# Performance work log

Measured on AMD Instinct MI355X. Metric: run time of the kernel, lower is better.

Reference implementation:

```python
import jax, jax.numpy as jnp
import numpy as np

LN_EPS = 1e-5
NEG_INF = -1e9

def _layer_norm(x, w, b):
    mu = jnp.mean(x, axis=-1, keepdims=True)
    var = jnp.mean(jnp.square(x - mu), axis=-1, keepdims=True)
    return (x - mu) * jax.lax.rsqrt(var + LN_EPS) * w + b

def _mha(q, k, v, wq, wk, wv, wo, mask, num_heads):
    # q: [B,Lq,D], k/v: [B,Lk,D]; weights stored as [in,out]
    B, Lq, D = q.shape
    Lk = k.shape[1]
    dh = D // num_heads
    Q = (q @ wq).reshape(B, Lq, num_heads, dh)
    K = (k @ wk).reshape(B, Lk, num_heads, dh)
    V = (v @ wv).reshape(B, Lk, num_heads, dh)
    scores = jnp.einsum('bqhd,bkhd->bhqk', Q, K) / jnp.sqrt(jnp.asarray(dh, q.dtype))
    if mask is not None:
        scores = jnp.where(mask, NEG_INF, scores)  # mask True = forbidden
    A = jax.nn.softmax(scores, axis=-1)
    out = jnp.einsum('bhqk,bkhd->bqhd', A, V).reshape(B, Lq, D)
    return out @ wo

def setup_inputs() -> dict:
    key = jax.random.key(0)
    B, L, Lm, D, F = 4, 1024, 1024, 1024, 4096
    ks = jax.random.split(key, 12)
    s = 0.02
    inp = {
        'tgt': jax.random.normal(ks[0], (B, L, D), jnp.float32),
        'memory': jax.random.normal(ks[1], (B, Lm, D), jnp.float32),
        'tgt_padding_mask': jnp.zeros((B, L), bool),
        'memory_padding_mask': jnp.zeros((B, Lm), bool),
        'sa_wq': jax.random.normal(ks[2], (D, D), jnp.float32) * s,
        'sa_wk': jax.random.normal(ks[3], (D, D), jnp.float32) * s,
        'sa_wv': jax.random.normal(ks[4], (D, D), jnp.float32) * s,
        'sa_wo': jax.random.normal(ks[5], (D, D), jnp.float32) * s,
        'ca_wq': jax.random.normal(ks[6], (D, D), jnp.float32) * s,
        'ca_wk': jax.random.normal(ks[7], (D, D), jnp.float32) * s,
        'ca_wv': jax.random.normal(ks[8], (D, D), jnp.float32) * s,
        'ca_wo': jax.random.normal(ks[9], (D, D), jnp.float32) * s,
        'ffn_w1': jax.random.normal(ks[10], (D, F), jnp.float32) * s,
        'ffn_b1': jnp.zeros((F,), jnp.float32),
        'ffn_w2': jax.random.normal(ks[11], (F, D), jnp.float32) * s,
        'ffn_b2': jnp.zeros((D,), jnp.float32),
        'ln1_w': jnp.ones((D,), jnp.float32), 'ln1_b': jnp.zeros((D,), jnp.float32),
        'ln2_w': jnp.ones((D,), jnp.float32), 'ln2_b': jnp.zeros((D,), jnp.float32),
        'ln3_w': jnp.ones((D,), jnp.float32), 'ln3_b': jnp.zeros((D,), jnp.float32),
    }
    return inp

def reference(tgt, memory, tgt_padding_mask, memory_padding_mask,
              sa_wq, sa_wk, sa_wv, sa_wo,
              ca_wq, ca_wk, ca_wv, ca_wo,
              ffn_w1, ffn_b1, ffn_w2, ffn_b2,
              ln1_w, ln1_b, ln2_w, ln2_b, ln3_w, ln3_b):
    NUM_HEADS = 16
    B, L, D = tgt.shape
    causal = jnp.triu(jnp.ones((L, L), bool), k=1)  # True = forbidden
    attn_mask = causal[None, None, :, :] | tgt_padding_mask[:, None, None, :]
    x = _mha(tgt, tgt, tgt, sa_wq, sa_wk, sa_wv, sa_wo, attn_mask, NUM_HEADS)
    tgt = _layer_norm(tgt + x, ln1_w, ln1_b)
    mem_mask = memory_padding_mask[:, None, None, :]
    x = _mha(tgt, memory, memory, ca_wq, ca_wk, ca_wv, ca_wo, mem_mask, NUM_HEADS)
    tgt = _layer_norm(tgt + x, ln2_w, ln2_b)
    h = jax.nn.gelu(tgt @ ffn_w1 + ffn_b1)
    ffn_out = h @ ffn_w2 + ffn_b2
    return _layer_norm(tgt + ffn_out, ln3_w, ln3_b)
```

## Files before the change

kernel.cpp:

```cpp
#include <hip/hip_runtime.h>
#include <cstdint>
#include <cstddef>


using u16 = unsigned short;
typedef float f32x4 __attribute__((ext_vector_type(4)));
typedef __bf16 bf16x8 __attribute__((ext_vector_type(8)));

__device__ inline float bf2f(u16 h) { return __uint_as_float(((unsigned)h) << 16); }
__device__ inline u16 f2bf(float f) {
  unsigned u = __float_as_uint(f);
  u += 0x7fffu + ((u >> 16) & 1u);
  return (u16)(u >> 16);
}

__device__ inline void gload16(const void* g, void* l) {
  __builtin_amdgcn_global_load_lds(
      (__attribute__((address_space(1))) void*)g,
      (__attribute__((address_space(3))) void*)l, 16, 0, 0);
}

template <int N>
__device__ inline void waitv() {
  if constexpr (N == 0)      asm volatile("s_waitcnt vmcnt(0)" ::: "memory");
  else if constexpr (N == 4) asm volatile("s_waitcnt vmcnt(4)" ::: "memory");
  else if constexpr (N == 6) asm volatile("s_waitcnt vmcnt(6)" ::: "memory");
  else if constexpr (N == 8) asm volatile("s_waitcnt vmcnt(8)" ::: "memory");
}
template <int N>
__device__ inline void waitl() {
  if constexpr (N == 0)      asm volatile("s_waitcnt lgkmcnt(0)" ::: "memory");
  else if constexpr (N == 4) asm volatile("s_waitcnt lgkmcnt(4)" ::: "memory");
  else if constexpr (N == 8) asm volatile("s_waitcnt lgkmcnt(8)" ::: "memory");
}
__device__ inline void sbar() {
  __builtin_amdgcn_s_barrier();
  __builtin_amdgcn_sched_barrier(0);
}

__device__ inline float gelu_tanh(float x) {
  float u = 0.7978845608028654f * (x + 0.044715f * x * x * x);
  u = fminf(fmaxf(u, -10.f), 10.f);
  float e = __expf(2.0f * u);
  float t = (e - 1.0f) / (e + 1.0f);
  return 0.5f * x * (1.0f + t);
}

__global__ __launch_bounds__(256) void fill_sentinel(float* __restrict__ out,
                                                     float val, int n) {
  int i = blockIdx.x * 1024 + threadIdx.x;
#pragma unroll
  for (int j = 0; j < 4; j++)
    if (i + j * 256 < n) out[i + j * 256] = val;
}

__global__ __launch_bounds__(256) void cast_bf16(const float* __restrict__ S,
                                                 u16* __restrict__ D) {
  int i = (blockIdx.x * 256 + threadIdx.x) * 8;
  float4 a = *(const float4*)&S[i];
  float4 b = *(const float4*)&S[i + 4];
  union { u16 h[8]; uint4 v; } p;
  p.h[0] = f2bf(a.x); p.h[1] = f2bf(a.y); p.h[2] = f2bf(a.z); p.h[3] = f2bf(a.w);
  p.h[4] = f2bf(b.x); p.h[5] = f2bf(b.y); p.h[6] = f2bf(b.z); p.h[7] = f2bf(b.w);
  *(uint4*)&D[i] = p.v;
}

__global__ __launch_bounds__(256) void transpose_w(const float* __restrict__ S,
                                                   u16* __restrict__ D, int K,
                                                   int N) {
  __shared__ float t[32][33];
  int bx = blockIdx.x * 32, by = blockIdx.y * 32;
  int tx = threadIdx.x & 31, ty = threadIdx.x >> 5;
  for (int i = ty; i < 32; i += 8)
    t[i][tx] = S[(size_t)(by + i) * N + bx + tx];
  __syncthreads();
  for (int i = ty; i < 32; i += 8)
    D[(size_t)(bx + i) * K + by + tx] = f2bf(t[tx][i]);
}

__global__ __launch_bounds__(256) void transpose_v(const u16* __restrict__ S,
                                                   int stride,
                                                   u16* __restrict__ VT, int L) {
  __shared__ u16 t[32][33];
  int bh = blockIdx.z, b = bh >> 4, h = bh & 15;
  int l0 = blockIdx.x * 32, d0 = blockIdx.y * 32;
  int tx = threadIdx.x & 31, ty = threadIdx.x >> 5;
  const u16* Sp = S + (size_t)(b * L) * stride + h * 64;
  for (int i = ty; i < 32; i += 8)
    t[i][tx] = Sp[(size_t)(l0 + i) * stride + d0 + tx];
  __syncthreads();
  for (int i = ty; i < 32; i += 8)
    VT[((size_t)bh * 64 + d0 + i) * L + l0 + tx] = t[tx][i];
}

template <int EPI>
__global__ __launch_bounds__(512) void gemm_8ph(
    const u16* __restrict__ A, int lda, const u16* __restrict__ Bt,
    u16* __restrict__ C, int ldc, const float* __restrict__ bias, int K) {
  constexpr int BK = 64;
  __shared__ __attribute__((aligned(16))) u16 As[2][256 * BK];
  __shared__ __attribute__((aligned(16))) u16 Bs[2][256 * BK];
  const int tid = threadIdx.x;
  const int lane = tid & 63, w = tid >> 6;
  const int wr = (w >> 2) * 128, wc = (w & 3) * 64;
  const int ml = lane & 15, quad = lane >> 4;

  const int nwg = gridDim.x * gridDim.y;
  const int orig = blockIdx.x + blockIdx.y * gridDim.x;
  const int wg = (orig & 7) * (nwg >> 3) + (orig >> 3);
  const int bx = wg % gridDim.x, by = wg / gridDim.x;
  const int bm = by * 256, bn = bx * 256;

  const u16* Bb = Bt + (size_t)bn * K;
  const int srow = tid >> 3;
  const int scol = ((tid & 7) ^ (srow & 7)) * 8;

  auto stgA = [&](int t, int h) {
    const int buf = t & 1, k0 = t * BK;
#pragma unroll
    for (int r = 0; r < 2; r++)
      gload16(&A[(size_t)(bm + h * 128 + r * 64 + srow) * lda + k0 + scol],
              &As[buf][(h * 128 + r * 64) * BK + w * 512]);
  };
  auto stgB = [&](int t, int h) {
    const int buf = t & 1, k0 = t * BK;
#pragma unroll
    for (int r = 0; r < 2; r++)
      gload16(&Bb[(size_t)(h * 128 + r * 64 + srow) * K + k0 + scol],
              &Bs[buf][(h * 128 + r * 64) * BK + w * 512]);
  };
  auto ldsA = [&](int buf, int row, int ks) -> bf16x8 {
    return *(const bf16x8*)&As[buf][row * BK + (((ks * 4 + quad) ^ (row & 7)) * 8)];
  };
  auto ldsB = [&](int buf, int row, int ks) -> bf16x8 {
    return *(const bf16x8*)&Bs[buf][row * BK + (((ks * 4 + quad) ^ (row & 7)) * 8)];
  };

  f32x4 acc[8][4] = {};
  const int nk = K / BK;

  stgA(0, 0); stgA(0, 1); stgB(0, 0); stgB(0, 1); stgA(1, 0); stgA(1, 1);
  waitv<4>();
  sbar();

  for (int t = 0; t < nk; t++) {
    const int cur = t & 1;
    bf16x8 aq0[8], aq1[8], bq[4];

#pragma unroll
    for (int i = 0; i < 4; i++)
#pragma unroll
      for (int ks = 0; ks < 2; ks++)
        aq0[i * 2 + ks] = ldsA(cur, wr + i * 16 + ml, ks);
#pragma unroll
    for (int j = 0; j < 2; j++)
#pragma unroll
      for (int ks = 0; ks < 2; ks++)
        bq[j * 2 + ks] = ldsB(cur, wc + j * 16 + ml, ks);
    if (t + 1 < nk) stgB(t + 1, 0);
    __builtin_amdgcn_s_barrier();
    waitl<0>();
    __builtin_amdgcn_sched_barrier(0);
    __builtin_amdgcn_s_setprio(1);
#pragma unroll
    for (int ks = 0; ks < 2; ks++)
#pragma unroll
      for (int i = 0; i < 4; i++)
#pragma unroll
        for (int j = 0; j < 2; j++)
          acc[i][j] = __builtin_amdgcn_mfma_f32_16x16x32_bf16(
              aq0[i * 2 + ks], bq[j * 2 + ks], acc[i][j], 0, 0, 0);
    __builtin_amdgcn_s_setprio(0);
    sbar();

#pragma unroll
    for (int i = 0; i < 4; i++)
#pragma unroll
      for (int ks = 0; ks < 2; ks++)
        aq1[i * 2 + ks] = ldsA(cur, wr + 64 + i * 16 + ml, ks);
    if (t + 1 < nk) stgB(t + 1, 1);
    __builtin_amdgcn_s_barrier();
    waitl<0>();
    __builtin_amdgcn_sched_barrier(0);
    __builtin_amdgcn_s_setprio(1);
#pragma unroll
    for (int ks = 0; ks < 2; ks++)
#pragma unroll
      for (int i = 0; i < 4; i++)
#pragma unroll
        for (int j = 0; j < 2; j++)
          acc[4 + i][j] = __builtin_amdgcn_mfma_f32_16x16x32_bf16(
              aq1[i * 2 + ks], bq[j * 2 + ks], acc[4 + i][j], 0, 0, 0);
    __builtin_amdgcn_s_setprio(0);
    sbar();

#pragma unroll
    for (int j = 0; j < 2; j++)
#pragma unroll
      for (int ks = 0; ks < 2; ks++)
        bq[j * 2 + ks] = ldsB(cur, wc + 32 + j * 16 + ml, ks);
    if (t + 2 < nk) stgA(t + 2, 0);
    __builtin_amdgcn_s_barrier();
    waitl<0>();
    __builtin_amdgcn_sched_barrier(0);
    __builtin_amdgcn_s_setprio(1);
#pragma unroll
    for (int ks = 0; ks < 2; ks++)
#pragma unroll
      for (int i = 0; i < 4; i++)
#pragma unroll
        for (int j = 0; j < 2; j++)
          acc[4 + i][2 + j] = __builtin_amdgcn_mfma_f32_16x16x32_bf16(
              aq1[i * 2 + ks], bq[j * 2 + ks], acc[4 + i][2 + j], 0, 0, 0);
    __builtin_amdgcn_s_setprio(0);
    sbar();

    if (t + 2 < nk) {
      stgA(t + 2, 1);
      waitv<4>();
    } else if (t + 1 < nk) {
      waitv<0>();
    }
    sbar();
    __builtin_amdgcn_s_setprio(1);
#pragma unroll
    for (int ks = 0; ks < 2; ks++)
#pragma unroll
      for (int i = 0; i < 4; i++)
#pragma unroll
        for (int j = 0; j < 2; j++)
          acc[i][2 + j] = __builtin_amdgcn_mfma_f32_16x16x32_bf16(
              aq0[i * 2 + ks], bq[j * 2 + ks], acc[i][2 + j], 0, 0, 0);
    __builtin_amdgcn_s_setprio(0);
    sbar();
  }

#pragma unroll
  for (int i = 0; i < 8; i++)
#pragma unroll
    for (int j = 0; j < 4; j++)
#pragma unroll
      for (int r = 0; r < 4; r++) {
        int row = bm + wr + i * 16 + quad * 4 + r;
        int col = bn + wc + j * 16 + ml;
        float v = acc[i][j][r];
        if (bias) v += bias[col];
        if (EPI == 1) v = gelu_tanh(v);
        C[(size_t)row * ldc + col] = f2bf(v);
      }
}

template <int EPI, int BM, int BN, int WM, int WN>
__global__ __launch_bounds__(512) void gemm_big(
    const u16* __restrict__ A, int lda, const u16* __restrict__ Bt,
    u16* __restrict__ C, int ldc, const float* __restrict__ bias, int K) {
  constexpr int BK = 64;
  constexpr int WTM = BM / WM, WTN = BN / WN;
  constexpr int MR = WTM / 16, NR = WTN / 16;
  constexpr int RPR = 64;
  constexpr int AR = BM / RPR, BR = BN / RPR;
  constexpr int GPT = AR + BR;
  __shared__ __attribute__((aligned(16))) u16 As[2][BM * BK];
  __shared__ __attribute__((aligned(16))) u16 Bs[2][BN * BK];
  const int tid = threadIdx.x;
  const int lane = tid & 63, w = tid >> 6;
  const int wr = (w / WN) * WTM, wc = (w % WN) * WTN;
  const int ml = lane & 15, quad = lane >> 4;

  const int nwg = gridDim.x * gridDim.y;
  const int orig = blockIdx.x + blockIdx.y * gridDim.x;
  const int wg = (orig & 7) * (nwg >> 3) + (orig >> 3);
  const int bx = wg % gridDim.x, by = wg / gridDim.x;
  const int bm = by * BM, bn = bx * BN;

  const u16* Bb = Bt + (size_t)bn * K;
  const int srow = tid >> 3;
  const int scol = ((tid & 7) ^ (srow & 7)) * 8;

  auto stage = [&](int t, int buf) {
    const int k0 = t * BK;
#pragma unroll
    for (int r = 0; r < AR; r++)
      gload16(&A[(size_t)(bm + r * RPR + srow) * lda + k0 + scol],
              &As[buf][r * RPR * BK + w * 512]);
#pragma unroll
    for (int r = 0; r < BR; r++)
      gload16(&Bb[(size_t)(r * RPR + srow) * K + k0 + scol],
              &Bs[buf][r * RPR * BK + w * 512]);
  };
  auto ldsA = [&](int buf, int row, int ks) -> bf16x8 {
    return *(const bf16x8*)&As[buf][row * BK + (((ks * 4 + quad) ^ (row & 7)) * 8)];
  };
  auto ldsB = [&](int buf, int row, int ks) -> bf16x8 {
    return *(const bf16x8*)&Bs[buf][row * BK + (((ks * 4 + quad) ^ (row & 7)) * 8)];
  };

  f32x4 acc[MR][NR] = {};
  const int nk = K / BK;
  stage(0, 0);
  for (int t = 0; t < nk; t++) {
    const int cur = t & 1;
    if (t + 1 < nk) {
      stage(t + 1, cur ^ 1);
      waitv<GPT>();
    } else {
      waitv<0>();
    }
    __builtin_amdgcn_s_barrier();
    __builtin_amdgcn_sched_barrier(0);

    bf16x8 af0[MR], af1[MR], bf0[NR], bf1[NR];
#pragma unroll
    for (int j = 0; j < NR; j++) bf0[j] = ldsB(cur, wc + j * 16 + ml, 0);
#pragma unroll
    for (int i = 0; i < MR; i++) af0[i] = ldsA(cur, wr + i * 16 + ml, 0);
#pragma unroll
    for (int j = 0; j < NR; j++) bf1[j] = ldsB(cur, wc + j * 16 + ml, 1);
#pragma unroll
    for (int i = 0; i < MR; i++) af1[i] = ldsA(cur, wr + i * 16 + ml, 1);
    waitl<MR + NR>();
    __builtin_amdgcn_sched_barrier(0);
    __builtin_amdgcn_s_setprio(1);
#pragma unroll
    for (int i = 0; i < MR; i++)
#pragma unroll
      for (int j = 0; j < NR; j++)
        acc[i][j] = __builtin_amdgcn_mfma_f32_16x16x32_bf16(af0[i], bf0[j], acc[i][j], 0, 0, 0);
    __builtin_amdgcn_s_setprio(0);
    waitl<0>();
    __builtin_amdgcn_sched_barrier(0);
    __builtin_amdgcn_s_setprio(1);
#pragma unroll
    for (int i = 0; i < MR; i++)
#pragma unroll
      for (int j = 0; j < NR; j++)
        acc[i][j] = __builtin_amdgcn_mfma_f32_16x16x32_bf16(af1[i], bf1[j], acc[i][j], 0, 0, 0);
    __builtin_amdgcn_s_setprio(0);

    __builtin_amdgcn_s_barrier();
    __builtin_amdgcn_sched_barrier(0);
  }

#pragma unroll
  for (int i = 0; i < MR; i++)
#pragma unroll
    for (int j = 0; j < NR; j++)
#pragma unroll
      for (int r = 0; r < 4; r++) {
        int row = bm + wr + i * 16 + quad * 4 + r;
        int col = bn + wc + j * 16 + ml;
        float v = acc[i][j][r];
        if (bias) v += bias[col];
        if (EPI == 1) v = gelu_tanh(v);
        C[(size_t)row * ldc + col] = f2bf(v);
      }
}

template <int EPI, int BN, int BK>
__global__ __launch_bounds__(256) void gemm_sm(
    const u16* __restrict__ A, int lda, const u16* __restrict__ Bt,
    u16* __restrict__ C, int ldc, const float* __restrict__ bias, int K) {
  constexpr int ACCN = BN / 32;
  constexpr int CPR = BK / 8, CM = CPR - 1;
  constexpr int RPR = 2048 / BK;
  constexpr int AR = 128 / RPR, BR = BN / RPR;
  __shared__ __attribute__((aligned(16))) u16 As[2][128 * BK];
  __shared__ __attribute__((aligned(16))) u16 Bs[2][BN * BK];
  const int tid = threadIdx.x;
  const int lane = tid & 63, w = tid >> 6;
  const int wr = (BN == 128) ? (w >> 1) * 64 : (w & 1) * 64;
  const int wc = (BN == 128) ? (w & 1) * 64 : (w >> 1) * 32;
  const int ml = lane & 15, quad = lane >> 4;

  const int nwg = gridDim.x * gridDim.y;
  const int orig = blockIdx.x + blockIdx.y * gridDim.x;
  const int wg = (orig & 7) * (nwg >> 3) + (orig >> 3);
  const int bx = wg % gridDim.x, by = wg / gridDim.x;
  const int bm = by * 128, bn = bx * BN;

  const u16* Bb = Bt + (size_t)bn * K;
  const int srow = tid / CPR;
  const int skey = ((srow * BK) >> 6) & CM;
  const int scol = ((tid % CPR) ^ skey) * 8;

  auto stage = [&](int k0, int buf) {
#pragma unroll
    for (int r = 0; r < AR; r++)
      gload16(&A[(size_t)(bm + r * RPR + srow) * lda + k0 + scol],
              &As[buf][r * RPR * BK + w * 512]);
#pragma unroll
    for (int r = 0; r < BR; r++)
      gload16(&Bb[(size_t)(r * RPR + srow) * K + k0 + scol],
              &Bs[buf][r * RPR * BK + w * 512]);
  };

  f32x4 acc[4][ACCN] = {};
  const int nk = K / BK;
  stage(0, 0);
  for (int t = 0; t < nk; t++) {
    const int cur = t & 1;
    __syncthreads();
    if (t + 1 < nk) stage((t + 1) * BK, cur ^ 1);
#pragma unroll
    for (int kk = 0; kk < BK; kk += 32) {
      bf16x8 af[4], bfr[ACCN];
#pragma unroll
      for (int i = 0; i < 4; i++) {
        const int row = wr + i * 16 + ml;
        const int p = ((quad + (kk >> 3)) ^ (((row * BK) >> 6) & CM)) * 8;
        af[i] = *(const bf16x8*)&As[cur][row * BK + p];
      }
#pragma unroll
      for (int j = 0; j < ACCN; j++) {
        const int row = wc + j * 16 + ml;
        const int p = ((quad + (kk >> 3)) ^ (((row * BK) >> 6) & CM)) * 8;
        bfr[j] = *(const bf16x8*)&Bs[cur][row * BK + p];
      }
#pragma unroll
      for (int i = 0; i < 4; i++)
#pragma unroll
        for (int j = 0; j < ACCN; j++)
          acc[i][j] = __builtin_amdgcn_mfma_f32_16x16x32_bf16(af[i], bfr[j],
                                                              acc[i][j], 0, 0, 0);
    }
  }

#pragma unroll
  for (int i = 0; i < 4; i++)
#pragma unroll
    for (int j = 0; j < ACCN; j++)
#pragma unroll
      for (int r = 0; r < 4; r++) {
        int row = bm + wr + i * 16 + quad * 4 + r;
        int col = bn + wc + j * 16 + ml;
        float v = acc[i][j][r];
        if (bias) v += bias[col];
        if (EPI == 1) v = gelu_tanh(v);
        C[(size_t)row * ldc + col] = f2bf(v);
      }
}

#define ATS 72
__global__ __launch_bounds__(256) void attn(
    const u16* __restrict__ Qb, int qstride, const u16* __restrict__ Kb,
    int kstride, const u16* __restrict__ VT, u16* __restrict__ Ob, int ostride,
    int L, int causal) {
  __shared__ __attribute__((aligned(16))) u16 Qs[64 * ATS];
  __shared__ __attribute__((aligned(16))) u16 Ks[64 * ATS];
  __shared__ __attribute__((aligned(16))) u16 Vs[64 * ATS];
  __shared__ __attribute__((aligned(16))) u16 Ps[4][16 * ATS];
  int tid = threadIdx.x, lane = tid & 63, w = tid >> 6;
  int ml = lane & 15, quad = lane >> 4;
  const int nwg = gridDim.x * gridDim.y;
  const int orig = blockIdx.x + blockIdx.y * gridDim.x;
  const int wg = (orig & 7) * (nwg >> 3) + (orig >> 3);
  int qt = wg % gridDim.x, bh = wg / gridDim.x;
  int b = bh >> 4, h = bh & 15;
  const u16* Qp = Qb + (size_t)(b * L) * qstride + h * 64;
  const u16* Kp = Kb + (size_t)(b * L) * kstride + h * 64;
  const u16* Vp = VT + (size_t)bh * 64 * L;

  {
    int r = tid >> 3, cg = (tid & 7) * 8;
    *(uint4*)&Qs[r * ATS + cg] =
        *(const uint4*)&Qp[(size_t)(qt * 64 + r) * qstride + cg];
    *(uint4*)&Qs[(r + 32) * ATS + cg] =
        *(const uint4*)&Qp[(size_t)(qt * 64 + r + 32) * qstride + cg];
  }

  const int r0 = tid >> 3, cg = (tid & 7) * 8;
  uint4 rk0, rk1, rv0, rv1;
  auto issueKV = [&](int kt) {
    rk0 = *(const uint4*)&Kp[(size_t)(kt * 64 + r0) * kstride + cg];
    rk1 = *(const uint4*)&Kp[(size_t)(kt * 64 + r0 + 32) * kstride + cg];
    rv0 = *(const uint4*)&Vp[(size_t)r0 * L + kt * 64 + cg];
    rv1 = *(const uint4*)&Vp[(size_t)(r0 + 32) * L + kt * 64 + cg];
  };
  auto storeKV = [&]() {
    *(uint4*)&Ks[r0 * ATS + cg] = rk0;
    *(uint4*)&Ks[(r0 + 32) * ATS + cg] = rk1;
    *(uint4*)&Vs[r0 * ATS + cg] = rv0;
    *(uint4*)&Vs[(r0 + 32) * ATS + cg] = rv1;
  };

  __syncthreads();
  bf16x8 aq0 = *(const bf16x8*)&Qs[(w * 16 + ml) * ATS + quad * 8];
  bf16x8 aq1 = *(const bf16x8*)&Qs[(w * 16 + ml) * ATS + 32 + quad * 8];

  float lrow[4] = {0.f, 0.f, 0.f, 0.f};
  f32x4 oacc[4] = {};
  int qbase = qt * 64 + w * 16 + quad * 4;

  int ktend = causal ? qt : (L / 64 - 1);
  issueKV(0);
  for (int kt = 0; kt <= ktend; kt++) {
    storeKV();
    __syncthreads();
    if (kt < ktend) issueKV(kt + 1);

    f32x4 sacc[4] = {};
#pragma unroll
    for (int t = 0; t < 4; t++) {
      bf16x8 bk0 = *(const bf16x8*)&Ks[(t * 16 + ml) * ATS + quad * 8];
      bf16x8 bk1 = *(const bf16x8*)&Ks[(t * 16 + ml) * ATS + 32 + quad * 8];
      sacc[t] = __builtin_amdgcn_mfma_f32_16x16x32_bf16(aq0, bk0, sacc[t], 0, 0, 0);
      sacc[t] = __builtin_amdgcn_mfma_f32_16x16x32_bf16(aq1, bk1, sacc[t], 0, 0, 0);
    }
#pragma unroll
    for (int t = 0; t < 4; t++)
#pragma unroll
      for (int r = 0; r < 4; r++) {
        bool masked = causal && (kt * 64 + t * 16 + ml > qbase + r);
        float p = masked ? 0.f : __expf(sacc[t][r] * 0.125f - 11.0f);
        sacc[t][r] = p;
        lrow[r] += p;
      }
    u16* Pw = &Ps[w][0];
#pragma unroll
    for (int t = 0; t < 4; t++)
#pragma unroll
      for (int r = 0; r < 4; r++)
        Pw[(quad * 4 + r) * ATS + t * 16 + ml] = f2bf(sacc[t][r]);
    __syncthreads();
    bf16x8 ap0 = *(const bf16x8*)&Pw[ml * ATS + quad * 8];
    bf16x8 ap1 = *(const bf16x8*)&Pw[ml * ATS + 32 + quad * 8];
#pragma unroll
    for (int t = 0; t < 4; t++) {
      bf16x8 bv0 = *(const bf16x8*)&Vs[(t * 16 + ml) * ATS + quad * 8];
      bf16x8 bv1 = *(const bf16x8*)&Vs[(t * 16 + ml) * ATS + 32 + quad * 8];
      oacc[t] = __builtin_amdgcn_mfma_f32_16x16x32_bf16(ap0, bv0, oacc[t], 0, 0, 0);
      oacc[t] = __builtin_amdgcn_mfma_f32_16x16x32_bf16(ap1, bv1, oacc[t], 0, 0, 0);
    }
    __syncthreads();
  }

#pragma unroll
  for (int r = 0; r < 4; r++) {
    float l = lrow[r];
    l += __shfl_xor(l, 1);
    l += __shfl_xor(l, 2);
    l += __shfl_xor(l, 4);
    l += __shfl_xor(l, 8);
    lrow[r] = l;
  }
#pragma unroll
  for (int r = 0; r < 4; r++) {
    float inv = 1.0f / fmaxf(lrow[r], 1e-37f);
#pragma unroll
    for (int t = 0; t < 4; t++)
      Ob[(size_t)(b * L + qbase + r) * ostride + h * 64 + t * 16 + ml] =
          f2bf(oacc[t][r] * inv);
  }
}

__global__ __launch_bounds__(256) void add_ln(
    const u16* __restrict__ base16, const float* __restrict__ base32,
    const u16* __restrict__ delta, const float* __restrict__ lw,
    const float* __restrict__ lb, u16* __restrict__ out16,
    float* __restrict__ out32) {
  const int D = 1024;
  int row = blockIdx.x;
  float v[4], s = 0.f, s2 = 0.f;
#pragma unroll
  for (int i = 0; i < 4; i++) {
    int c = threadIdx.x + i * 256;
    size_t idx = (size_t)row * D + c;
    float bse = base32 ? base32[idx] : bf2f(base16[idx]);
    float x = bse + bf2f(delta[idx]);
    v[i] = x; s += x; s2 += x * x;
  }
  for (int off = 32; off >= 1; off >>= 1) {
    s += __shfl_xor(s, off);
    s2 += __shfl_xor(s2, off);
  }
  __shared__ float red[8];
  int wid = threadIdx.x >> 6, lane = threadIdx.x & 63;
  if (lane == 0) { red[wid] = s; red[4 + wid] = s2; }
  __syncthreads();
  s = red[0] + red[1] + red[2] + red[3];
  s2 = red[4] + red[5] + red[6] + red[7];
  float mu = s * (1.0f / 1024.0f);
  float var = s2 * (1.0f / 1024.0f) - mu * mu;
  float rs = rsqrtf(fmaxf(var, 0.f) + 1e-5f);
#pragma unroll
  for (int i = 0; i < 4; i++) {
    int c = threadIdx.x + i * 256;
    size_t idx = (size_t)row * D + c;
    float y = (v[i] - mu) * rs * lw[c] + lb[c];
    if (out16) out16[idx] = f2bf(y);
    if (out32) out32[idx] = y;
  }
}

extern "C" void kernel_launch(void* const* d_in, const int* in_sizes, int n_in,
                              void* d_out, int out_size, void* d_ws,
                              size_t ws_size, hipStream_t stream) {
  const int L = 1024;
  const size_t MB = 1ull << 20;
  dim3 blk(256);
  dim3 blk512(512);

  if (ws_size < 64 * MB) {
    fill_sentinel<<<(out_size + 1023) / 1024, blk, 0, stream>>>(
        (float*)d_out, 1000.0f + (float)(ws_size >> 20), out_size);
    return;
  }

  const float* tgt = (const float*)d_in[0];
  const float* memv = (const float*)d_in[1];
  const float* sa_wq = (const float*)d_in[4];
  const float* sa_wk = (const float*)d_in[5];
  const float* sa_wv = (const float*)d_in[6];
  const float* sa_wo = (const float*)d_in[7];
  const float* ca_wq = (const float*)d_in[8];
  const float* ca_wk = (const float*)d_in[9];
  const float* ca_wv = (const float*)d_in[10];
  const float* ca_wo = (const float*)d_in[11];
  const float* ffn_w1 = (const float*)d_in[12];
  const float* ffn_b1 = (const float*)d_in[13];
  const float* ffn_w2 = (const float*)d_in[14];
  const float* ffn_b2 = (const float*)d_in[15];
  const float* ln1w = (const float*)d_in[16];
  const float* ln1b = (const float*)d_in[17];
  const float* ln2w = (const float*)d_in[18];
  const float* ln2b = (const float*)d_in[19];
  const float* ln3w = (const float*)d_in[20];
  const float* ln3b = (const float*)d_in[21];

  const size_t Mu = 1024 * 1024;
  char* base = (char*)d_ws;
  u16* Wt = (u16*)base;
  u16* sa_qkv_t = Wt;
  u16* sa_o_t = Wt + 3 * Mu;
  u16* ca_q_t = Wt + 4 * Mu;
  u16* ca_kv_t = Wt + 5 * Mu;
  u16* ca_o_t = Wt + 7 * Mu;
  u16* ffn1_t = Wt;
  u16* ffn2_t = Wt + 4 * Mu;
  u16* QKV = (u16*)(base + 16 * MB);
  u16* Qca = (u16*)(base + 16 * MB);
  u16* KVca = (u16*)(base + 24 * MB);
  u16* T2b = (u16*)(base + 16 * MB);
  u16* Hb = (u16*)(base + 24 * MB);
  u16* VTb = (u16*)(base + 40 * MB);
  u16* mem_b = (u16*)(base + 40 * MB);
  u16* tgt_b = (u16*)(base + 48 * MB);
  u16* PROJ = (u16*)(base + 48 * MB);
  u16* T1b = (u16*)(base + 56 * MB);
  u16* PROJ2 = (u16*)(base + 56 * MB);

  transpose_w<<<dim3(32, 32), blk, 0, stream>>>(sa_wq, sa_qkv_t, 1024, 1024);
  transpose_w<<<dim3(32, 32), blk, 0, stream>>>(sa_wk, sa_qkv_t + Mu, 1024, 1024);
  transpose_w<<<dim3(32, 32), blk, 0, stream>>>(sa_wv, sa_qkv_t + 2 * Mu, 1024, 1024);
  transpose_w<<<dim3(32, 32), blk, 0, stream>>>(sa_wo, sa_o_t, 1024, 1024);
  transpose_w<<<dim3(32, 32), blk, 0, stream>>>(ca_wq, ca_q_t, 1024, 1024);
  transpose_w<<<dim3(32, 32), blk, 0, stream>>>(ca_wk, ca_kv_t, 1024, 1024);
  transpose_w<<<dim3(32, 32), blk, 0, stream>>>(ca_wv, ca_kv_t + Mu, 1024, 1024);
  transpose_w<<<dim3(32, 32), blk, 0, stream>>>(ca_wo, ca_o_t, 1024, 1024);

  cast_bf16<<<2048, blk, 0, stream>>>(tgt, tgt_b);
  gemm_8ph<0><<<dim3(12, 16), blk512, 0, stream>>>(
      tgt_b, 1024, sa_qkv_t, QKV, 3072, nullptr, 1024);
  transpose_v<<<dim3(32, 2, 64), blk, 0, stream>>>(QKV + 2048, 3072, VTb, L);
  attn<<<dim3(16, 64), blk, 0, stream>>>(QKV, 3072, QKV + 1024, 3072, VTb, QKV, 3072, L, 1);
  cast_bf16<<<2048, blk, 0, stream>>>(memv, mem_b);
  gemm_sm<0, 64, 64><<<dim3(16, 32), blk, 0, stream>>>(
      QKV, 3072, sa_o_t, PROJ, 1024, nullptr, 1024);
  add_ln<<<4096, blk, 0, stream>>>(nullptr, tgt, PROJ, ln1w, ln1b, T1b, nullptr);

  gemm_sm<0, 64, 64><<<dim3(16, 32), blk, 0, stream>>>(
      T1b, 1024, ca_q_t, Qca, 1024, nullptr, 1024);
  gemm_big<0, 128, 256, 2, 4><<<dim3(8, 32), blk512, 0, stream>>>(
      mem_b, 1024, ca_kv_t, KVca, 2048, nullptr, 1024);
  transpose_v<<<dim3(32, 2, 64), blk, 0, stream>>>(KVca + 1024, 2048, VTb, L);
  attn<<<dim3(16, 64), blk, 0, stream>>>(Qca, 1024, KVca, 2048, VTb, Qca, 1024, L, 0);
  gemm_sm<0, 64, 64><<<dim3(16, 32), blk, 0, stream>>>(
      Qca, 1024, ca_o_t, PROJ, 1024, nullptr, 1024);
  transpose_w<<<dim3(128, 32), blk, 0, stream>>>(ffn_w1, ffn1_t, 1024, 4096);
  transpose_w<<<dim3(32, 128), blk, 0, stream>>>(ffn_w2, ffn2_t, 4096, 1024);
  add_ln<<<4096, blk, 0, stream>>>(T1b, nullptr, PROJ, ln2w, ln2b, T2b, nullptr);

  gemm_8ph<1><<<dim3(16, 16), blk512, 0, stream>>>(
      T2b, 1024, ffn1_t, Hb, 4096, ffn_b1, 1024);
  gemm_sm<0, 64, 64><<<dim3(16, 32), blk, 0, stream>>>(
      Hb, 4096, ffn2_t, PROJ2, 1024, ffn_b2, 4096);
  add_ln<<<4096, blk, 0, stream>>>(T2b, nullptr, PROJ2, ln3w, ln3b, nullptr, (float*)d_out);
}
```

Measured before the change: 547.6 us.

## Replace GEMM kernels with BK=32 vmcnt-pipelined kernel and batch weight transposes

```diff
diff --git a/kernel.cpp b/kernel.cpp
--- a/kernel.cpp
+++ b/kernel.cpp
@@ -23,6 +23,7 @@
 template <int N>
 __device__ inline void waitv() {
   if constexpr (N == 0)      asm volatile("s_waitcnt vmcnt(0)" ::: "memory");
+  else if constexpr (N == 3) asm volatile("s_waitcnt vmcnt(3)" ::: "memory");
   else if constexpr (N == 4) asm volatile("s_waitcnt vmcnt(4)" ::: "memory");
   else if constexpr (N == 6) asm volatile("s_waitcnt vmcnt(6)" ::: "memory");
   else if constexpr (N == 8) asm volatile("s_waitcnt vmcnt(8)" ::: "memory");
@@ -76,6 +77,28 @@
   __syncthreads();
   for (int i = ty; i < 32; i += 8)
     D[(size_t)(bx + i) * K + by + tx] = f2bf(t[tx][i]);
+}
+
+__global__ __launch_bounds__(256) void transpose_w8(
+    const float* s0, const float* s1, const float* s2, const float* s3,
+    const float* s4, const float* s5, const float* s6, const float* s7,
+    u16* __restrict__ D) {
+  const float* S;
+  switch (blockIdx.z) {
+    case 0: S = s0; break; case 1: S = s1; break;
+    case 2: S = s2; break; case 3: S = s3; break;
+    case 4: S = s4; break; case 5: S = s5; break;
+    case 6: S = s6; break; default: S = s7; break;
+  }
+  u16* Dp = D + (size_t)blockIdx.z * (1024 * 1024);
+  __shared__ float t[32][33];
+  int bx = blockIdx.x * 32, by = blockIdx.y * 32;
+  int tx = threadIdx.x & 31, ty = threadIdx.x >> 5;
+  for (int i = ty; i < 32; i += 8)
+    t[i][tx] = S[(size_t)(by + i) * 1024 + bx + tx];
+  __syncthreads();
+  for (int i = ty; i < 32; i += 8)
+    Dp[(size_t)(bx + i) * 1024 + by + tx] = f2bf(t[tx][i]);
 }
 
 __global__ __launch_bounds__(256) void transpose_v(const u16* __restrict__ S,
@@ -250,52 +273,45 @@
       }
 }
 
-template <int EPI, int BM, int BN, int WM, int WN>
-__global__ __launch_bounds__(512) void gemm_big(
+template <int EPI, int BN>
+__global__ __launch_bounds__(256) void gemm_cv(
     const u16* __restrict__ A, int lda, const u16* __restrict__ Bt,
     u16* __restrict__ C, int ldc, const float* __restrict__ bias, int K) {
-  constexpr int BK = 64;
-  constexpr int WTM = BM / WM, WTN = BN / WN;
-  constexpr int MR = WTM / 16, NR = WTN / 16;
-  constexpr int RPR = 64;
-  constexpr int AR = BM / RPR, BR = BN / RPR;
+  constexpr int BK = 32;
+  constexpr int NR = (BN == 128) ? 4 : 2;
+  constexpr int AR = 2, BR = BN / 64;
   constexpr int GPT = AR + BR;
-  __shared__ __attribute__((aligned(16))) u16 As[2][BM * BK];
+  __shared__ __attribute__((aligned(16))) u16 As[2][128 * BK];
   __shared__ __attribute__((aligned(16))) u16 Bs[2][BN * BK];
   const int tid = threadIdx.x;
   const int lane = tid & 63, w = tid >> 6;
-  const int wr = (w / WN) * WTM, wc = (w % WN) * WTN;
+  const int wr = (BN == 128) ? (w >> 1) * 64 : (w & 1) * 64;
+  const int wc = (BN == 128) ? (w & 1) * 64 : (w >> 1) * 32;
   const int ml = lane & 15, quad = lane >> 4;
 
   const int nwg = gridDim.x * gridDim.y;
   const int orig = blockIdx.x + blockIdx.y * gridDim.x;
   const int wg = (orig & 7) * (nwg >> 3) + (orig >> 3);
   const int bx = wg % gridDim.x, by = wg / gridDim.x;
-  const int bm = by * BM, bn = bx * BN;
+  const int bm = by * 128, bn = bx * BN;
 
   const u16* Bb = Bt + (size_t)bn * K;
-  const int srow = tid >> 3;
-  const int scol = ((tid & 7) ^ (srow & 7)) * 8;
+  const int srow = tid >> 2;
+  const int scol = ((tid & 3) ^ ((srow >> 1) & 3)) * 8;
 
   auto stage = [&](int t, int buf) {
     const int k0 = t * BK;
 #pragma unroll
     for (int r = 0; r < AR; r++)
-      gload16(&A[(size_t)(bm + r * RPR + srow) * lda + k0 + scol],
-              &As[buf][r * RPR * BK + w * 512]);
+      gload16(&A[(size_t)(bm + r * 64 + srow) * lda + k0 + scol],
+              &As[buf][r * 64 * BK + w * 512]);
 #pragma unroll
     for (int r = 0; r < BR; r++)
-      gload16(&Bb[(size_t)(r * RPR + srow) * K + k0 + scol],
-              &Bs[buf][r * RPR * BK + w * 512]);
+      gload16(&Bb[(size_t)(r * 64 + srow) * K + k0 + scol],
+              &Bs[buf][r * 64 * BK + w * 512]);
   };
-  auto ldsA = [&](int buf, int row, int ks) -> bf16x8 {
-    return *(const bf16x8*)&As[buf][row * BK + (((ks * 4 + quad) ^ (row & 7)) * 8)];
-  };
-  auto ldsB = [&](int buf, int row, int ks) -> bf16x8 {
-    return *(const bf16x8*)&Bs[buf][row * BK + (((ks * 4 + quad) ^ (row & 7)) * 8)];
-  };
-
-  f32x4 acc[MR][NR] = {};
+
+  f32x4 acc[4][NR] = {};
   const int nk = K / BK;
   stage(0, 0);
   for (int t = 0; t < nk; t++) {
@@ -309,126 +325,33 @@
     __builtin_amdgcn_s_barrier();
     __builtin_amdgcn_sched_barrier(0);
 
-    bf16x8 af0[MR], af1[MR], bf0[NR], bf1[NR];
-#pragma unroll
-    for (int j = 0; j < NR; j++) bf0[j] = ldsB(cur, wc + j * 16 + ml, 0);
-#pragma unroll
-    for (int i = 0; i < MR; i++) af0[i] = ldsA(cur, wr + i * 16 + ml, 0);
-#pragma unroll
-    for (int j = 0; j < NR; j++) bf1[j] = ldsB(cur, wc + j * 16 + ml, 1);
-#pragma unroll
-    for (int i = 0; i < MR; i++) af1[i] = ldsA(cur, wr + i * 16 + ml, 1);
-    waitl<MR + NR>();
-    __builtin_amdgcn_sched_barrier(0);
+    bf16x8 af[4], bfr[NR];
+#pragma unroll
+    for (int i = 0; i < 4; i++) {
+      const int row = wr + i * 16 + ml;
+      af[i] = *(const bf16x8*)&As[cur][row * BK + ((quad ^ ((row >> 1) & 3)) * 8)];
+    }
+#pragma unroll
+    for (int j = 0; j < NR; j++) {
+      const int row = wc + j * 16 + ml;
+      bfr[j] = *(const bf16x8*)&Bs[cur][row * BK + ((quad ^ ((row >> 1) & 3)) * 8)];
+    }
     __builtin_amdgcn_s_setprio(1);
 #pragma unroll
-    for (int i = 0; i < MR; i++)
+    for (int i = 0; i < 4; i++)
 #pragma unroll
       for (int j = 0; j < NR; j++)
-        acc[i][j] = __builtin_amdgcn_mfma_f32_16x16x32_bf16(af0[i], bf0[j], acc[i][j], 0, 0, 0);
+        acc[i][j] = __builtin_amdgcn_mfma_f32_16x16x32_bf16(af[i], bfr[j],
+                                                            acc[i][j], 0, 0, 0);
     __builtin_amdgcn_s_setprio(0);
-    waitl<0>();
-    __builtin_amdgcn_sched_barrier(0);
-    __builtin_amdgcn_s_setprio(1);
-#pragma unroll
-    for (int i = 0; i < MR; i++)
-#pragma unroll
-      for (int j = 0; j < NR; j++)
-        acc[i][j] = __builtin_amdgcn_mfma_f32_16x16x32_bf16(af1[i], bf1[j], acc[i][j], 0, 0, 0);
-    __builtin_amdgcn_s_setprio(0);
-
     __builtin_amdgcn_s_barrier();
     __builtin_amdgcn_sched_barrier(0);
   }
 
 #pragma unroll
-  for (int i = 0; i < MR; i++)
+  for (int i = 0; i < 4; i++)
 #pragma unroll
     for (int j = 0; j < NR; j++)
-#pragma unroll
-      for (int r = 0; r < 4; r++) {
-        int row = bm + wr + i * 16 + quad * 4 + r;
-        int col = bn + wc + j * 16 + ml;
-        float v = acc[i][j][r];
-        if (bias) v += bias[col];
-        if (EPI == 1) v = gelu_tanh(v);
-        C[(size_t)row * ldc + col] = f2bf(v);
-      }
-}
-
-template <int EPI, int BN, int BK>
-__global__ __launch_bounds__(256) void gemm_sm(
-    const u16* __restrict__ A, int lda, const u16* __restrict__ Bt,
-    u16* __restrict__ C, int ldc, const float* __restrict__ bias, int K) {
-  constexpr int ACCN = BN / 32;
-  constexpr int CPR = BK / 8, CM = CPR - 1;
-  constexpr int RPR = 2048 / BK;
-  constexpr int AR = 128 / RPR, BR = BN / RPR;
-  __shared__ __attribute__((aligned(16))) u16 As[2][128 * BK];
-  __shared__ __attribute__((aligned(16))) u16 Bs[2][BN * BK];
-  const int tid = threadIdx.x;
-  const int lane = tid & 63, w = tid >> 6;
-  const int wr = (BN == 128) ? (w >> 1) * 64 : (w & 1) * 64;
-  const int wc = (BN == 128) ? (w & 1) * 64 : (w >> 1) * 32;
-  const int ml = lane & 15, quad = lane >> 4;
-
-  const int nwg = gridDim.x * gridDim.y;
-  const int orig = blockIdx.x + blockIdx.y * gridDim.x;
-  const int wg = (orig & 7) * (nwg >> 3) + (orig >> 3);
-  const int bx = wg % gridDim.x, by = wg / gridDim.x;
-  const int bm = by * 128, bn = bx * BN;
-
-  const u16* Bb = Bt + (size_t)bn * K;
-  const int srow = tid / CPR;
-  const int skey = ((srow * BK) >> 6) & CM;
-  const int scol = ((tid % CPR) ^ skey) * 8;
-
-  auto stage = [&](int k0, int buf) {
-#pragma unroll
-    for (int r = 0; r < AR; r++)
-      gload16(&A[(size_t)(bm + r * RPR + srow) * lda + k0 + scol],
-              &As[buf][r * RPR * BK + w * 512]);
-#pragma unroll
-    for (int r = 0; r < BR; r++)
-      gload16(&Bb[(size_t)(r * RPR + srow) * K + k0 + scol],
-              &Bs[buf][r * RPR * BK + w * 512]);
-  };
-
-  f32x4 acc[4][ACCN] = {};
-  const int nk = K / BK;
-  stage(0, 0);
-  for (int t = 0; t < nk; t++) {
-    const int cur = t & 1;
-    __syncthreads();
-    if (t + 1 < nk) stage((t + 1) * BK, cur ^ 1);
-#pragma unroll
-    for (int kk = 0; kk < BK; kk += 32) {
-      bf16x8 af[4], bfr[ACCN];
-#pragma unroll
-      for (int i = 0; i < 4; i++) {
-        const int row = wr + i * 16 + ml;
-        const int p = ((quad + (kk >> 3)) ^ (((row * BK) >> 6) & CM)) * 8;
-        af[i] = *(const bf16x8*)&As[cur][row * BK + p];
-      }
-#pragma unroll
-      for (int j = 0; j < ACCN; j++) {
-        const int row = wc + j * 16 + ml;
-        const int p = ((quad + (kk >> 3)) ^ (((row * BK) >> 6) & CM)) * 8;
-        bfr[j] = *(const bf16x8*)&Bs[cur][row * BK + p];
-      }
-#pragma unroll
-      for (int i = 0; i < 4; i++)
-#pragma unroll
-        for (int j = 0; j < ACCN; j++)
-          acc[i][j] = __builtin_amdgcn_mfma_f32_16x16x32_bf16(af[i], bfr[j],
-                                                              acc[i][j], 0, 0, 0);
-    }
-  }
-
-#pragma unroll
-  for (int i = 0; i < 4; i++)
-#pragma unroll
-    for (int j = 0; j < ACCN; j++)
 #pragma unroll
       for (int r = 0; r < 4; r++) {
         int row = bm + wr + i * 16 + quad * 4 + r;
@@ -649,14 +572,8 @@
   u16* T1b = (u16*)(base + 56 * MB);
   u16* PROJ2 = (u16*)(base + 56 * MB);
 
-  transpose_w<<<dim3(32, 32), blk, 0, stream>>>(sa_wq, sa_qkv_t, 1024, 1024);
-  transpose_w<<<dim3(32, 32), blk, 0, stream>>>(sa_wk, sa_qkv_t + Mu, 1024, 1024);
-  transpose_w<<<dim3(32, 32), blk, 0, stream>>>(sa_wv, sa_qkv_t + 2 * Mu, 1024, 1024);
-  transpose_w<<<dim3(32, 32), blk, 0, stream>>>(sa_wo, sa_o_t, 1024, 1024);
-  transpose_w<<<dim3(32, 32), blk, 0, stream>>>(ca_wq, ca_q_t, 1024, 1024);
-  transpose_w<<<dim3(32, 32), blk, 0, stream>>>(ca_wk, ca_kv_t, 1024, 1024);
-  transpose_w<<<dim3(32, 32), blk, 0, stream>>>(ca_wv, ca_kv_t + Mu, 1024, 1024);
-  transpose_w<<<dim3(32, 32), blk, 0, stream>>>(ca_wo, ca_o_t, 1024, 1024);
+  transpose_w8<<<dim3(32, 32, 8), blk, 0, stream>>>(
+      sa_wq, sa_wk, sa_wv, sa_wo, ca_wq, ca_wk, ca_wv, ca_wo, Wt);
 
   cast_bf16<<<2048, blk, 0, stream>>>(tgt, tgt_b);
   gemm_8ph<0><<<dim3(12, 16), blk512, 0, stream>>>(
@@ -664,17 +581,17 @@
   transpose_v<<<dim3(32, 2, 64), blk, 0, stream>>>(QKV + 2048, 3072, VTb, L);
   attn<<<dim3(16, 64), blk, 0, stream>>>(QKV, 3072, QKV + 1024, 3072, VTb, QKV, 3072, L, 1);
   cast_bf16<<<2048, blk, 0, stream>>>(memv, mem_b);
-  gemm_sm<0, 64, 64><<<dim3(16, 32), blk, 0, stream>>>(
+  gemm_cv<0, 64><<<dim3(16, 32), blk, 0, stream>>>(
       QKV, 3072, sa_o_t, PROJ, 1024, nullptr, 1024);
   add_ln<<<4096, blk, 0, stream>>>(nullptr, tgt, PROJ, ln1w, ln1b, T1b, nullptr);
 
-  gemm_sm<0, 64, 64><<<dim3(16, 32), blk, 0, stream>>>(
+  gemm_cv<0, 64><<<dim3(16, 32), blk, 0, stream>>>(
       T1b, 1024, ca_q_t, Qca, 1024, nullptr, 1024);
-  gemm_big<0, 128, 256, 2, 4><<<dim3(8, 32), blk512, 0, stream>>>(
+  gemm_cv<0, 128><<<dim3(16, 32), blk, 0, stream>>>(
       mem_b, 1024, ca_kv_t, KVca, 2048, nullptr, 1024);
   transpose_v<<<dim3(32, 2, 64), blk, 0, stream>>>(KVca + 1024, 2048, VTb, L);
   attn<<<dim3(16, 64), blk, 0, stream>>>(Qca, 1024, KVca, 2048, VTb, Qca, 1024, L, 0);
-  gemm_sm<0, 64, 64><<<dim3(16, 32), blk, 0, stream>>>(
+  gemm_cv<0, 64><<<dim3(16, 32), blk, 0, stream>>>(
       Qca, 1024, ca_o_t, PROJ, 1024, nullptr, 1024);
   transpose_w<<<dim3(128, 32), blk, 0, stream>>>(ffn_w1, ffn1_t, 1024, 4096);
   transpose_w<<<dim3(32, 128), blk, 0, stream>>>(ffn_w2, ffn2_t, 4096, 1024);
@@ -682,7 +599,7 @@
 
   gemm_8ph<1><<<dim3(16, 16), blk512, 0, stream>>>(
       T2b, 1024, ffn1_t, Hb, 4096, ffn_b1, 1024);
-  gemm_sm<0, 64, 64><<<dim3(16, 32), blk, 0, stream>>>(
+  gemm_cv<0, 64><<<dim3(16, 32), blk, 0, stream>>>(
       Hb, 4096, ffn2_t, PROJ2, 1024, ffn_b2, 4096);
   add_ln<<<4096, blk, 0, stream>>>(T2b, nullptr, PROJ2, ln3w, ln3b, nullptr, (float*)d_out);
 }
```

Result: no change. 556.8 us (+1.7%).
